# Kernel optimization log

Measured on AMD Instinct MI355X. Metric: run time of the kernel, lower is better.

## Reference

```python
import jax, jax.numpy as jnp
import numpy as np

B, S, E, H = 64, 256, 1024, 16
D = E // H  # head dim = 64


def setup_inputs() -> dict:
    key = jax.random.key(0)
    ks = jax.random.split(key, 6)
    x = jax.random.normal(ks[0], (B, S, E), dtype=jnp.float32)
    # torch nn.MultiheadAttention packed in-projection [3E, E] and biases
    sc = 1.0 / np.sqrt(E)
    in_proj_w = jax.random.normal(ks[1], (3 * E, E), dtype=jnp.float32) * sc
    in_proj_b = jax.random.normal(ks[2], (3 * E,), dtype=jnp.float32) * 0.02
    out_proj_w = jax.random.normal(ks[3], (E, E), dtype=jnp.float32) * sc
    out_proj_b = jax.random.normal(ks[4], (E,), dtype=jnp.float32) * 0.02
    # spatial bias = exp(-dist^2 / (2*median)) in (0, 1], symmetric
    pos = jax.random.normal(ks[5], (S, 3), dtype=jnp.float32)
    dist = jnp.sqrt(jnp.sum((pos[:, None, :] - pos[None, :, :]) ** 2, -1) + 1e-12)
    med = jnp.median(dist)
    spatial_bias = jnp.exp(-dist ** 2 / (2.0 * med))
    return {"x": x, "in_proj_w": in_proj_w, "in_proj_b": in_proj_b,
            "out_proj_w": out_proj_w, "out_proj_b": out_proj_b,
            "spatial_bias": spatial_bias}


def reference(x, in_proj_w, in_proj_b, out_proj_w, out_proj_b, spatial_bias):
    # packed QKV projection: x [B,S,E] @ in_proj_w.T [E,3E]
    qkv = x @ in_proj_w.T + in_proj_b          # [B,S,3E]
    q, k, v = jnp.split(qkv, 3, axis=-1)       # each [B,S,E]
    q = q.reshape(B, S, H, D)
    k = k.reshape(B, S, H, D)
    v = v.reshape(B, S, H, D)
    scale = 1.0 / jnp.sqrt(jnp.asarray(D, dtype=x.dtype))
    # additive float attn_mask broadcast over batch & heads
    scores = jnp.einsum('bqhd,bkhd->bhqk', q, k) * scale + spatial_bias[None, None]
    attn = jax.nn.softmax(scores, axis=-1)     # [B,H,S,S]
    ctx = jnp.einsum('bhqk,bkhd->bqhd', attn, v).reshape(B, S, E)
    h = ctx @ out_proj_w.T + out_proj_b        # [B,S,E]
    return x + h
```

## Files before the change

### kernel.cpp

```cpp
#include <hip/hip_runtime.h>
#include <hip/hip_bf16.h>
#include <stdint.h>


typedef __attribute__((ext_vector_type(8))) __bf16 bf16x8;
typedef __attribute__((ext_vector_type(4))) float f32x4;

#define DEVI static __device__ __forceinline__

DEVI unsigned short f2bf(float f) {
  union { float f; unsigned u; } x; x.f = f;
  unsigned r = x.u + 0x7fffu + ((x.u >> 16) & 1u);
  return (unsigned short)(r >> 16);
}

DEVI float bf2f(unsigned short h) {
  union { unsigned u; float f; } x; x.u = (unsigned)h << 16; return x.f;
}

typedef unsigned int __attribute__((address_space(1))) u32_g;
typedef unsigned int __attribute__((address_space(3))) u32_l;

DEVI void g2l16(const unsigned short* g, unsigned short* l) {
  __builtin_amdgcn_global_load_lds((const u32_g*)g, (u32_l*)l, 16, 0, 0);
}

__global__ __launch_bounds__(256) void cvt_kernel(const float* __restrict__ s,
                                                  unsigned short* __restrict__ d, int n) {
  int i = (blockIdx.x * 256 + threadIdx.x) * 4;
  if (i >= n) return;
  float4 v = *(const float4*)(s + i);
  ushort4 o;
  o.x = f2bf(v.x); o.y = f2bf(v.y); o.z = f2bf(v.z); o.w = f2bf(v.w);
  *(ushort4*)(d + i) = o;
}

template <int EPI>
__global__ __launch_bounds__(256, 2)
void gemm4(const unsigned short* __restrict__ A,
           const unsigned short* __restrict__ Bw,
           const float* __restrict__ bias,
           unsigned short* __restrict__ Qo,
           unsigned short* __restrict__ Ko,
           unsigned short* __restrict__ VTo,
           const float* __restrict__ Xres,
           float* __restrict__ Out) {
  extern __shared__ unsigned short lds[];
  const int lane = threadIdx.x & 63, wid = threadIdx.x >> 6;
  const int l15 = lane & 15, lg = lane >> 4;
  const int wr = wid >> 1, wcn = wid & 1;
  const int am0 = blockIdx.x * 256, bn0 = blockIdx.y * 128;

  const int srow0 = wid * 16 + (lane >> 2);
  const int scb0  = (lane & 3) * 16;

  f32x4 acc[8][4] = {};
  bf16x8 a[8], b[4];

#define SWZ(row) ((((row) >> 1) & 3) << 4)
#define VMC(N) asm volatile("s_waitcnt vmcnt(" #N ")" ::: "memory")

#define STAGE(s) { \
    const int slot_ = (s) % 3; \
    _Pragma("unroll") \
    for (int j = 0; j < 4; ++j) { \
      const int row_ = j * 64 + srow0; \
      const int cs_ = scb0 ^ SWZ(row_); \
      g2l16(A + (size_t)(am0 + row_) * 1024 + (s) * 32 + (cs_ >> 1), \
            &lds[slot_ * 12288 + (j * 64 + wid * 16) * 32]); \
    } \
    _Pragma("unroll") \
    for (int j = 0; j < 2; ++j) { \
      const int row_ = j * 64 + srow0; \
      const int cs_ = scb0 ^ SWZ(row_); \
      g2l16(Bw + (size_t)(bn0 + row_) * 1024 + (s) * 32 + (cs_ >> 1), \
            &lds[slot_ * 12288 + 8192 + (j * 64 + wid * 16) * 32]); \
    } }

#define LOADF(p) { \
    const unsigned short* As_ = &lds[((p) % 3) * 12288]; \
    const unsigned short* Bs_ = As_ + 8192; \
    _Pragma("unroll") \
    for (int mf = 0; mf < 8; ++mf) { \
      const int row_ = wr * 128 + mf * 16 + l15; \
      a[mf] = *(const bf16x8*)((const char*)As_ + row_ * 64 + ((lg * 16) ^ SWZ(row_))); \
    } \
    _Pragma("unroll") \
    for (int nf = 0; nf < 4; ++nf) { \
      const int row_ = wcn * 64 + nf * 16 + l15; \
      b[nf] = *(const bf16x8*)((const char*)Bs_ + row_ * 64 + ((lg * 16) ^ SWZ(row_))); \
    } }

#define MM() { \
    __builtin_amdgcn_s_setprio(1); \
    _Pragma("unroll") \
    for (int mf = 0; mf < 8; ++mf) \
      _Pragma("unroll") \
      for (int nf = 0; nf < 4; ++nf) \
        acc[mf][nf] = __builtin_amdgcn_mfma_f32_16x16x32_bf16(a[mf], b[nf], acc[mf][nf], 0, 0, 0); \
    __builtin_amdgcn_s_setprio(0); }

  STAGE(0) STAGE(1)
  VMC(6);

#pragma unroll 1
  for (int p = 0; p < 32; ++p) {
    __builtin_amdgcn_s_barrier();
    if (p < 30) STAGE(p + 2)
    LOADF(p)
    asm volatile("s_waitcnt lgkmcnt(0)" ::: "memory");
    __builtin_amdgcn_sched_barrier(0);
    MM()
    if (p < 29) { VMC(6); } else { VMC(0); }
  }

  if (EPI == 0) {
#pragma unroll
    for (int nf = 0; nf < 4; ++nf) {
      const int col = bn0 + wcn * 64 + nf * 16 + l15;
      const int which = col >> 10;
      const int e = col & 1023;
      const int hh = e >> 6, dd = e & 63;
      const float bv = bias[col];
#pragma unroll
      for (int mf = 0; mf < 8; ++mf) {
        const int row0 = am0 + wr * 128 + mf * 16 + lg * 4;
        const int bb = row0 >> 8;
        const int s0 = row0 & 255;
        if (which == 2) {
          unsigned long long pk = 0;
#pragma unroll
          for (int r = 0; r < 4; ++r)
            pk |= (unsigned long long)f2bf(acc[mf][nf][r] + bv) << (16 * r);
          *(unsigned long long*)&VTo[((size_t)(bb * 16 + hh) * 64 + dd) * 256 + s0] = pk;
        } else if (which == 0) {
#pragma unroll
          for (int r = 0; r < 4; ++r)
            Qo[((size_t)(bb * 16 + hh) * 256 + s0 + r) * 64 + dd] = f2bf((acc[mf][nf][r] + bv) * 0.125f);
        } else {
#pragma unroll
          for (int r = 0; r < 4; ++r)
            Ko[((size_t)(bb * 16 + hh) * 256 + s0 + r) * 64 + dd] = f2bf(acc[mf][nf][r] + bv);
        }
      }
    }
  } else {
#pragma unroll
    for (int nf = 0; nf < 4; ++nf) {
      const int col = bn0 + wcn * 64 + nf * 16 + l15;
      const float bv = bias[col];
#pragma unroll
      for (int mf = 0; mf < 8; ++mf) {
#pragma unroll
        for (int r = 0; r < 4; ++r) {
          const int row = am0 + wr * 128 + mf * 16 + lg * 4 + r;
          const size_t idx = (size_t)row * 1024 + col;
          Out[idx] = Xres[idx] + acc[mf][nf][r] + bv;
        }
      }
    }
  }
#undef SWZ
#undef VMC
#undef STAGE
#undef LOADF
#undef MM
}

__global__ __launch_bounds__(256, 2)
void attn_kernel(const unsigned short* __restrict__ Qg,
                 const unsigned short* __restrict__ Kg,
                 const unsigned short* __restrict__ VTg,
                 const unsigned short* __restrict__ biasbf,
                 unsigned short* __restrict__ ctx) {
  __shared__ unsigned short Ks[256 * 64];
  __shared__ unsigned short P[4][64][40];
  const int lane = threadIdx.x & 63, wave = threadIdx.x >> 6;
  const int l15 = lane & 15, lg = lane >> 4;
  const int bh = blockIdx.x;
  const int bb = bh >> 4, hh = bh & 15;
  const size_t base = (size_t)bh * (256 * 64);
  const int q0 = wave * 64;

#pragma unroll
  for (int j = 0; j < 8; ++j) {
    const int r0 = (wave * 8 + j) * 8;
    const int row = r0 + (lane >> 3);
    const int gsrc = (lane & 7) ^ (row & 7);
    g2l16(&Kg[base + (size_t)row * 64 + gsrc * 8], &Ks[r0 * 64]);
  }
  asm volatile("s_waitcnt vmcnt(0)" ::: "memory");
  __builtin_amdgcn_sched_barrier(0);
  __builtin_amdgcn_s_barrier();

  bf16x8 qfr[4][2];
#pragma unroll
  for (int qi = 0; qi < 4; ++qi)
#pragma unroll
    for (int kc = 0; kc < 2; ++kc)
      qfr[qi][kc] = *(const bf16x8*)&Qg[base + (size_t)(q0 + qi * 16 + l15) * 64 + kc * 32 + lg * 8];

  f32x4 o[4][4] = {};
  float mrow[4], lrow[4];
#pragma unroll
  for (int i = 0; i < 4; ++i) { mrow[i] = -1e30f; lrow[i] = 0.f; }

#pragma unroll 1
  for (int c = 0; c < 8; ++c) {
    const int ck = c * 32;
    bf16x8 vb[4];
#pragma unroll
    for (int df = 0; df < 4; ++df)
      vb[df] = *(const bf16x8*)&VTg[base + (size_t)(df * 16 + l15) * 256 + ck + lg * 8];
    ushort4 bbf[2][4];
#pragma unroll
    for (int kr = 0; kr < 2; ++kr)
#pragma unroll
      for (int qi = 0; qi < 4; ++qi)
        bbf[kr][qi] = *(const ushort4*)&biasbf[(q0 + qi * 16 + l15) * 256 + ck + kr * 16 + lg * 4];
    bf16x8 kf[2][2];
#pragma unroll
    for (int kr = 0; kr < 2; ++kr)
#pragma unroll
      for (int kc = 0; kc < 2; ++kc) {
        const int row = ck + kr * 16 + l15;
        const int g = (kc * 4 + lg) ^ (row & 7);
        kf[kr][kc] = *(const bf16x8*)&Ks[row * 64 + g * 8];
      }
    f32x4 s[2][4] = {};
#pragma unroll
    for (int kr = 0; kr < 2; ++kr)
#pragma unroll
      for (int qi = 0; qi < 4; ++qi)
#pragma unroll
        for (int kc = 0; kc < 2; ++kc)
          s[kr][qi] = __builtin_amdgcn_mfma_f32_16x16x32_bf16(kf[kr][kc], qfr[qi][kc], s[kr][qi], 0, 0, 0);

    float cmax[4];
#pragma unroll
    for (int qi = 0; qi < 4; ++qi) cmax[qi] = -1e30f;
#pragma unroll
    for (int kr = 0; kr < 2; ++kr)
#pragma unroll
      for (int qi = 0; qi < 4; ++qi) {
        const unsigned short* bp = (const unsigned short*)&bbf[kr][qi];
#pragma unroll
        for (int r = 0; r < 4; ++r) {
          float v = s[kr][qi][r] + bf2f(bp[r]);
          s[kr][qi][r] = v;
          cmax[qi] = fmaxf(cmax[qi], v);
        }
      }
#pragma unroll
    for (int qi = 0; qi < 4; ++qi) {
      cmax[qi] = fmaxf(cmax[qi], __shfl_xor(cmax[qi], 16, 64));
      cmax[qi] = fmaxf(cmax[qi], __shfl_xor(cmax[qi], 32, 64));
    }
    int defer = 1;
#pragma unroll
    for (int qi = 0; qi < 4; ++qi) defer &= (cmax[qi] - mrow[qi] <= 8.f);
    const int full = !__all(defer);
    float resc[4];
#pragma unroll
    for (int qi = 0; qi < 4; ++qi) {
      if (full) {
        float mn = fmaxf(mrow[qi], cmax[qi]);
        resc[qi] = __expf(mrow[qi] - mn);
        mrow[qi] = mn;
      } else resc[qi] = 1.f;
    }
    float csum[4];
#pragma unroll
    for (int qi = 0; qi < 4; ++qi) csum[qi] = 0.f;
#pragma unroll
    for (int kr = 0; kr < 2; ++kr)
#pragma unroll
      for (int qi = 0; qi < 4; ++qi)
#pragma unroll
        for (int r = 0; r < 4; ++r) {
          float e = __expf(s[kr][qi][r] - mrow[qi]);
          s[kr][qi][r] = e;
          csum[qi] += e;
        }
#pragma unroll
    for (int qi = 0; qi < 4; ++qi) {
      csum[qi] += __shfl_xor(csum[qi], 16, 64);
      csum[qi] += __shfl_xor(csum[qi], 32, 64);
      lrow[qi] = lrow[qi] * resc[qi] + csum[qi];
    }
#pragma unroll
    for (int kr = 0; kr < 2; ++kr)
#pragma unroll
      for (int qi = 0; qi < 4; ++qi) {
        unsigned long long pk = 0;
#pragma unroll
        for (int r = 0; r < 4; ++r)
          pk |= (unsigned long long)f2bf(s[kr][qi][r]) << (16 * r);
        *(unsigned long long*)&P[wave][qi * 16 + l15][kr * 16 + lg * 4] = pk;
      }
    asm volatile("s_waitcnt lgkmcnt(0)" ::: "memory");
    if (full) {
#pragma unroll
      for (int qrf = 0; qrf < 4; ++qrf)
#pragma unroll
        for (int r = 0; r < 4; ++r) {
          float f = __shfl(resc[qrf], lg * 4 + r, 64);
#pragma unroll
          for (int df = 0; df < 4; ++df) o[qrf][df][r] *= f;
        }
    }
    bf16x8 pa[4];
#pragma unroll
    for (int qrf = 0; qrf < 4; ++qrf)
      pa[qrf] = *(const bf16x8*)&P[wave][qrf * 16 + l15][lg * 8];
#pragma unroll
    for (int qrf = 0; qrf < 4; ++qrf)
#pragma unroll
      for (int df = 0; df < 4; ++df)
        o[qrf][df] = __builtin_amdgcn_mfma_f32_16x16x32_bf16(pa[qrf], vb[df], o[qrf][df], 0, 0, 0);
  }

#pragma unroll
  for (int qrf = 0; qrf < 4; ++qrf)
#pragma unroll
    for (int r = 0; r < 4; ++r) {
      float li = __shfl(lrow[qrf], lg * 4 + r, 64);
      float inv = 1.0f / li;
      const int q = q0 + qrf * 16 + lg * 4 + r;
#pragma unroll
      for (int df = 0; df < 4; ++df) {
        const int d = df * 16 + l15;
        ctx[((size_t)(bb * 256 + q) * 16 + hh) * 64 + d] = f2bf(o[qrf][df][r] * inv);
      }
    }
}

extern "C" void kernel_launch(void* const* d_in, const int* in_sizes, int n_in,
                              void* d_out, int out_size, void* d_ws, size_t ws_size,
                              hipStream_t stream) {
  const float* x  = (const float*)d_in[0];
  const float* wi = (const float*)d_in[1];
  const float* bi = (const float*)d_in[2];
  const float* wo = (const float*)d_in[3];
  const float* bo = (const float*)d_in[4];
  const float* sb = (const float*)d_in[5];
  float* out = (float*)d_out;

  char* ws = (char*)d_ws;
  unsigned short* xbf  = (unsigned short*)(ws);
  unsigned short* winb = (unsigned short*)(ws + 33554432u);
  unsigned short* wob  = (unsigned short*)(ws + 39845888u);
  unsigned short* Qb   = (unsigned short*)(ws + 41943040u);
  unsigned short* Kb   = (unsigned short*)(ws + 75497472u);
  unsigned short* VTb  = (unsigned short*)(ws + 109051904u);
  unsigned short* ctx  = xbf;
  unsigned short* sbbf = winb;

  (void)hipFuncSetAttribute(reinterpret_cast<const void*>(gemm4<0>),
                            hipFuncAttributeMaxDynamicSharedMemorySize, 73728);
  (void)hipFuncSetAttribute(reinterpret_cast<const void*>(gemm4<1>),
                            hipFuncAttributeMaxDynamicSharedMemorySize, 73728);

  cvt_kernel<<<16384, 256, 0, stream>>>(x, xbf, 16777216);
  cvt_kernel<<<3072, 256, 0, stream>>>(wi, winb, 3145728);
  cvt_kernel<<<1024, 256, 0, stream>>>(wo, wob, 1048576);

  gemm4<0><<<dim3(64, 24), 256, 73728, stream>>>(xbf, winb, bi, Qb, Kb, VTb, nullptr, nullptr);

  cvt_kernel<<<64, 256, 0, stream>>>(sb, sbbf, 65536);

  attn_kernel<<<1024, 256, 0, stream>>>(Qb, Kb, VTb, sbbf, ctx);

  gemm4<1><<<dim3(64, 8), 256, 73728, stream>>>(ctx, wob, bo, nullptr, nullptr, nullptr, x, out);
}
```

Measured before the change: 286.4 us.

## Switch GEMMs to 8-wave 256x256 tiles with ping-pong LDS pipeline

Replaces the 4-wave 256x128-tile GEMM with an 8-wave 256x256-tile kernel that uses a 64-wide K step and double-buffered 128KB LDS. Global-to-LDS staging is interleaved in quarter-tile chunks between MFMA groups, with barriers separating the phases. The aim is higher arithmetic intensity per LDS byte and better overlap of loads with MFMA. In exchange, occupancy drops to one block per CU, the grid shrinks, and there are many more barriers.

```diff
diff --git a/kernel.cpp b/kernel.cpp
--- a/kernel.cpp
+++ b/kernel.cpp
@@ -36,83 +36,99 @@
 }
 
 template <int EPI>
-__global__ __launch_bounds__(256, 2)
-void gemm4(const unsigned short* __restrict__ A,
-           const unsigned short* __restrict__ Bw,
-           const float* __restrict__ bias,
-           unsigned short* __restrict__ Qo,
-           unsigned short* __restrict__ Ko,
-           unsigned short* __restrict__ VTo,
-           const float* __restrict__ Xres,
-           float* __restrict__ Out) {
+__global__ __launch_bounds__(512, 1)
+void gemm8p(const unsigned short* __restrict__ A,
+            const unsigned short* __restrict__ Bw,
+            const float* __restrict__ bias,
+            unsigned short* __restrict__ Qo,
+            unsigned short* __restrict__ Ko,
+            unsigned short* __restrict__ VTo,
+            const float* __restrict__ Xres,
+            float* __restrict__ Out) {
   extern __shared__ unsigned short lds[];
   const int lane = threadIdx.x & 63, wid = threadIdx.x >> 6;
   const int l15 = lane & 15, lg = lane >> 4;
-  const int wr = wid >> 1, wcn = wid & 1;
-  const int am0 = blockIdx.x * 256, bn0 = blockIdx.y * 128;
-
-  const int srow0 = wid * 16 + (lane >> 2);
-  const int scb0  = (lane & 3) * 16;
+  const int wr = wid >> 2, wcn = wid & 3;
+  const int am0 = blockIdx.x * 256, bn0 = blockIdx.y * 256;
+
+  const int sr = wid * 8 + (lane >> 3);
+  const int sg = lane & 7;
 
   f32x4 acc[8][4] = {};
-  bf16x8 a[8], b[4];
-
-#define SWZ(row) ((((row) >> 1) & 3) << 4)
+  bf16x8 a[4][2], b0[2][2], b1[2][2];
+
 #define VMC(N) asm volatile("s_waitcnt vmcnt(" #N ")" ::: "memory")
-
-#define STAGE(s) { \
-    const int slot_ = (s) % 3; \
-    _Pragma("unroll") \
-    for (int j = 0; j < 4; ++j) { \
-      const int row_ = j * 64 + srow0; \
-      const int cs_ = scb0 ^ SWZ(row_); \
-      g2l16(A + (size_t)(am0 + row_) * 1024 + (s) * 32 + (cs_ >> 1), \
-            &lds[slot_ * 12288 + (j * 64 + wid * 16) * 32]); \
-    } \
+#define LGKM() asm volatile("s_waitcnt lgkmcnt(0)" ::: "memory")
+#define BARR() __builtin_amdgcn_s_barrier()
+#define SW(r) (((r) >> 1) & 7)
+
+#define STG(OP, KT, HALF) { \
     _Pragma("unroll") \
     for (int j = 0; j < 2; ++j) { \
-      const int row_ = j * 64 + srow0; \
-      const int cs_ = scb0 ^ SWZ(row_); \
-      g2l16(Bw + (size_t)(bn0 + row_) * 1024 + (s) * 32 + (cs_ >> 1), \
-            &lds[slot_ * 12288 + 8192 + (j * 64 + wid * 16) * 32]); \
+      const int rin_ = j * 64 + sr; \
+      const int gs_ = sg ^ SW(rin_); \
+      const unsigned short* src_ = ((OP) ? Bw + (size_t)(bn0 + (HALF) * 128 + rin_) * 1024 \
+                                         : A  + (size_t)(am0 + (HALF) * 128 + rin_) * 1024) \
+                                   + (KT) * 64 + gs_ * 8; \
+      g2l16(src_, &lds[((KT) & 1) * 32768 + (OP) * 16384 + (HALF) * 8192 + (j * 64 + wid * 8) * 64]); \
     } }
 
-#define LOADF(p) { \
-    const unsigned short* As_ = &lds[((p) % 3) * 12288]; \
-    const unsigned short* Bs_ = As_ + 8192; \
+#define RDA(KT, HA) { \
+    const unsigned short* r_ = &lds[((KT) & 1) * 32768 + wr * 8192]; \
     _Pragma("unroll") \
-    for (int mf = 0; mf < 8; ++mf) { \
-      const int row_ = wr * 128 + mf * 16 + l15; \
-      a[mf] = *(const bf16x8*)((const char*)As_ + row_ * 64 + ((lg * 16) ^ SWZ(row_))); \
-    } \
+    for (int mfi = 0; mfi < 4; ++mfi) { \
+      const int rin_ = (HA) * 64 + mfi * 16 + l15; \
+      _Pragma("unroll") \
+      for (int kk = 0; kk < 2; ++kk) \
+        a[mfi][kk] = *(const bf16x8*)&r_[rin_ * 64 + ((kk * 4 + lg) ^ SW(rin_)) * 8]; \
+    } }
+
+#define RDB(BF, KT, HB) { \
+    const unsigned short* r_ = &lds[((KT) & 1) * 32768 + 16384 + (wcn >> 1) * 8192]; \
     _Pragma("unroll") \
-    for (int nf = 0; nf < 4; ++nf) { \
-      const int row_ = wcn * 64 + nf * 16 + l15; \
-      b[nf] = *(const bf16x8*)((const char*)Bs_ + row_ * 64 + ((lg * 16) ^ SWZ(row_))); \
+    for (int nfi = 0; nfi < 2; ++nfi) { \
+      const int rin_ = (wcn & 1) * 64 + (HB) * 32 + nfi * 16 + l15; \
+      _Pragma("unroll") \
+      for (int kk = 0; kk < 2; ++kk) \
+        BF[nfi][kk] = *(const bf16x8*)&r_[rin_ * 64 + ((kk * 4 + lg) ^ SW(rin_)) * 8]; \
     } }
 
-#define MM() { \
+#define MM(BF, HA, HB) { \
     __builtin_amdgcn_s_setprio(1); \
     _Pragma("unroll") \
-    for (int mf = 0; mf < 8; ++mf) \
+    for (int mfi = 0; mfi < 4; ++mfi) \
       _Pragma("unroll") \
-      for (int nf = 0; nf < 4; ++nf) \
-        acc[mf][nf] = __builtin_amdgcn_mfma_f32_16x16x32_bf16(a[mf], b[nf], acc[mf][nf], 0, 0, 0); \
+      for (int nfi = 0; nfi < 2; ++nfi) \
+        _Pragma("unroll") \
+        for (int kk = 0; kk < 2; ++kk) \
+          acc[(HA) * 4 + mfi][(HB) * 2 + nfi] = __builtin_amdgcn_mfma_f32_16x16x32_bf16( \
+              a[mfi][kk], BF[nfi][kk], acc[(HA) * 4 + mfi][(HB) * 2 + nfi], 0, 0, 0); \
     __builtin_amdgcn_s_setprio(0); }
 
-  STAGE(0) STAGE(1)
-  VMC(6);
+  STG(0, 0, 0) STG(0, 0, 1) STG(1, 0, 0) STG(1, 0, 1)
+  STG(1, 1, 0) STG(1, 1, 1) STG(0, 1, 0)
+  VMC(6); BARR();
 
 #pragma unroll 1
-  for (int p = 0; p < 32; ++p) {
-    __builtin_amdgcn_s_barrier();
-    if (p < 30) STAGE(p + 2)
-    LOADF(p)
-    asm volatile("s_waitcnt lgkmcnt(0)" ::: "memory");
-    __builtin_amdgcn_sched_barrier(0);
-    MM()
-    if (p < 29) { VMC(6); } else { VMC(0); }
+  for (int i = 0; i < 7; ++i) {
+    const int k0 = 2 * i, k1 = 2 * i + 1;
+    RDA(k0, 0) RDB(b0, k0, 0) STG(0, k1, 1)              BARR(); LGKM(); MM(b0, 0, 0) BARR();
+    RDB(b1, k0, 1)                                       BARR(); LGKM(); MM(b1, 0, 1) BARR();
+    RDA(k0, 1)                STG(1, k0 + 2, 0)          BARR(); LGKM(); MM(b1, 1, 1) BARR();
+    STG(1, k0 + 2, 1) STG(0, k0 + 2, 0)          VMC(6); BARR();         MM(b0, 1, 0) BARR();
+    RDA(k1, 0) RDB(b0, k1, 0) STG(0, k0 + 2, 1)          BARR(); LGKM(); MM(b0, 0, 0) BARR();
+    RDB(b1, k1, 1)                                       BARR(); LGKM(); MM(b1, 0, 1) BARR();
+    RDA(k1, 1)                STG(1, k1 + 2, 0)          BARR(); LGKM(); MM(b1, 1, 1) BARR();
+    STG(1, k1 + 2, 1) STG(0, k1 + 2, 0)          VMC(6); BARR();         MM(b0, 1, 0) BARR();
   }
+  RDA(14, 0) RDB(b0, 14, 0) STG(0, 15, 1)                BARR(); LGKM(); MM(b0, 0, 0) BARR();
+  RDB(b1, 14, 1)                                         BARR(); LGKM(); MM(b1, 0, 1) BARR();
+  RDA(14, 1)                                             BARR(); LGKM(); MM(b1, 1, 1) BARR();
+                                               VMC(0);   BARR();         MM(b0, 1, 0) BARR();
+  RDA(15, 0) RDB(b0, 15, 0)                              BARR(); LGKM(); MM(b0, 0, 0) BARR();
+  RDB(b1, 15, 1)                                         BARR(); LGKM(); MM(b1, 0, 1) BARR();
+  RDA(15, 1)                                             BARR(); LGKM(); MM(b1, 1, 1) BARR();
+                                                                         MM(b0, 1, 0)
 
   if (EPI == 0) {
 #pragma unroll
@@ -160,10 +176,13 @@
       }
     }
   }
-#undef SWZ
 #undef VMC
-#undef STAGE
-#undef LOADF
+#undef LGKM
+#undef BARR
+#undef SW
+#undef STG
+#undef RDA
+#undef RDB
 #undef MM
 }
 
@@ -356,20 +375,20 @@
   unsigned short* ctx  = xbf;
   unsigned short* sbbf = winb;
 
-  (void)hipFuncSetAttribute(reinterpret_cast<const void*>(gemm4<0>),
-                            hipFuncAttributeMaxDynamicSharedMemorySize, 73728);
-  (void)hipFuncSetAttribute(reinterpret_cast<const void*>(gemm4<1>),
-                            hipFuncAttributeMaxDynamicSharedMemorySize, 73728);
+  (void)hipFuncSetAttribute(reinterpret_cast<const void*>(gemm8p<0>),
+                            hipFuncAttributeMaxDynamicSharedMemorySize, 131072);
+  (void)hipFuncSetAttribute(reinterpret_cast<const void*>(gemm8p<1>),
+                            hipFuncAttributeMaxDynamicSharedMemorySize, 131072);
 
   cvt_kernel<<<16384, 256, 0, stream>>>(x, xbf, 16777216);
   cvt_kernel<<<3072, 256, 0, stream>>>(wi, winb, 3145728);
   cvt_kernel<<<1024, 256, 0, stream>>>(wo, wob, 1048576);
 
-  gemm4<0><<<dim3(64, 24), 256, 73728, stream>>>(xbf, winb, bi, Qb, Kb, VTb, nullptr, nullptr);
+  gemm8p<0><<<dim3(64, 12), 512, 131072, stream>>>(xbf, winb, bi, Qb, Kb, VTb, nullptr, nullptr);
 
   cvt_kernel<<<64, 256, 0, stream>>>(sb, sbbf, 65536);
 
   attn_kernel<<<1024, 256, 0, stream>>>(Qb, Kb, VTb, sbbf, ctx);
 
-  gemm4<1><<<dim3(64, 8), 256, 73728, stream>>>(ctx, wob, bo, nullptr, nullptr, nullptr, x, out);
-}
+  gemm8p<1><<<dim3(64, 4), 512, 131072, stream>>>(ctx, wob, bo, nullptr, nullptr, nullptr, x, out);
+}
```

After: 285.3 us. No clear change (-0.4%).
